# Performance work log

Measured on AMD Instinct MI355X. Metric: run time of the kernel, lower is better.

## Reference

```python
import jax, jax.numpy as jnp
import numpy as np

N_USERS = 100000
N_ITEMS = 50000
N_NODES = N_USERS + N_ITEMS  # 150000
N_EDGES = 1000000
N_INTENTS = 4
EMBED_K = 64
CHUNK = EMBED_K // N_INTENTS  # 16
N_LAYERS = 3


def setup_inputs() -> dict:
    key = jax.random.key(0)
    k1, k2, k3, k4 = jax.random.split(key, 4)
    Gu = jax.random.normal(k1, (N_USERS, EMBED_K), dtype=jnp.float32) * 0.1
    Gi = jax.random.normal(k2, (N_ITEMS, EMBED_K), dtype=jnp.float32) * 0.1
    edge_index = jax.random.randint(k3, (2, N_EDGES), 0, N_NODES, dtype=jnp.int64)
    edge_index_intents = jax.random.normal(k4, (N_INTENTS, N_EDGES), dtype=jnp.float32)
    return {"Gu": Gu, "Gi": Gi, "edge_index": edge_index,
            "edge_index_intents": edge_index_intents}


def dgcf_layer(x, row, col, edge_index_intents):
    # x: [N, K, C]; edge_index_intents: [K, E]
    w = jax.nn.softmax(edge_index_intents, axis=0).T  # [E, K]
    deg = (jax.ops.segment_sum(w, row, num_segments=N_NODES)
           + jax.ops.segment_sum(w, col, num_segments=N_NODES))  # [N, K]
    # deg^-0.5 with inf -> 0 (as in the torch code)
    dis = jnp.where(deg > 0, 1.0 / jnp.sqrt(jnp.maximum(deg, 1e-12)), 0.0)  # [N, K]
    norm = dis[row] * dis[col]  # [E, K]
    msg = norm[:, :, None] * x[row]  # [E, K, C] gather-multiply
    return jax.ops.segment_sum(msg, col, num_segments=N_NODES)  # scatter-add at targets


def reference(Gu, Gi, edge_index, edge_index_intents):
    row, col = edge_index[0], edge_index[1]
    # ego embeddings split into intent chunks: [N, K, C]
    x = jnp.concatenate([Gu, Gi], axis=0).reshape(N_NODES, N_INTENTS, CHUNK)
    for _ in range(N_LAYERS):
        x = dgcf_layer(x, row, col, edge_index_intents)
    return x
```

## Files before the change

### kernel.cpp

```cpp
#include <hip/hip_runtime.h>
#include <hip/hip_bf16.h>
#include <hip/hip_fp16.h>
#include <math.h>

#define N_USERS 100000
#define N_ITEMS 50000
#define N_NODES 150000
#define N_EDGES 1000000
#define N_GU_FLAT (N_USERS * 64)
#define N_ALL_FLAT (N_NODES * 64)
#define NBUCK 586
#define HPITCH (2 * NBUCK)
#define EPB 4096
#define NEB ((N_EDGES + EPB - 1) / EPB)
#define BCAP 2048
#define FIXS 16777216.0f

typedef __hip_bfloat16 bf16;
typedef unsigned short ushort_t;
typedef unsigned int uint_t;
typedef unsigned long long u64_t;

__device__ __forceinline__ ushort_t f2bs(float f) {
    bf16 h = __float2bfloat16(f);
    return *reinterpret_cast<ushort_t*>(&h);
}
__device__ __forceinline__ float lo2f(uint_t u) {
    float f; *reinterpret_cast<uint_t*>(&f) = u << 16; return f;
}
__device__ __forceinline__ float hi2f(uint_t u) {
    float f; *reinterpret_cast<uint_t*>(&f) = u & 0xFFFF0000u; return f;
}
__device__ __forceinline__ uint_t pack2(float a, float b) {
    return (uint_t)f2bs(a) | ((uint_t)f2bs(b) << 16);
}
__device__ __forceinline__ ushort_t f2hs(float f) {
    __half h = __float2half(f);
    return *reinterpret_cast<ushort_t*>(&h);
}
__device__ __forceinline__ float hs2f(ushort_t u) {
    __half h; *reinterpret_cast<ushort_t*>(&h) = u;
    return __half2float(h);
}
__device__ __forceinline__ int fix24(float w) {
    return (int)__float2int_rn(w * FIXS);
}

__global__ __launch_bounds__(1024) void s1_hist_cast(
        const int* __restrict__ ei,
        const float* __restrict__ Gu, const float* __restrict__ Gi,
        ushort_t* __restrict__ xG, uint_t* __restrict__ H, int gE) {
    int b = blockIdx.x;
    int t = threadIdx.x;
    if (b >= gE) {
        long base = ((long)(b - gE) * 1024 + t) * 4;
        if (base >= N_ALL_FLAT) return;
        float4 v = (base < N_GU_FLAT) ? *(const float4*)(Gu + base)
                                      : *(const float4*)(Gi + (base - N_GU_FLAT));
        uint2 o;
        o.x = pack2(v.x, v.y);
        o.y = pack2(v.z, v.w);
        *(uint2*)(xG + base) = o;
        return;
    }
    __shared__ uint_t h[HPITCH];
    for (int j = t; j < HPITCH; j += 1024) h[j] = 0;
    __syncthreads();
    int eb = b * EPB;
    int lim = min(EPB, N_EDGES - eb);
    for (int i = t; i < lim; i += 1024) {
        int e = eb + i;
        int r = ei[e];
        int c = ei[N_EDGES + e];
        atomicAdd(&h[c >> 8], 1u);
        atomicAdd(&h[NBUCK + (r >> 8)], 1u);
    }
    __syncthreads();
    for (int j = t; j < HPITCH; j += 1024) H[(size_t)b * HPITCH + j] = h[j];
}

__global__ __launch_bounds__(256) void s2_scan_blocks(
        const uint_t* __restrict__ H, uint_t* __restrict__ bases,
        uint_t* __restrict__ totals) {
    int j = blockIdx.x;
    int t = threadIdx.x;
    __shared__ uint_t s[256];
    uint_t v = (t < NEB) ? H[(size_t)t * HPITCH + j] : 0u;
    s[t] = v;
    __syncthreads();
    for (int off = 1; off < 256; off <<= 1) {
        uint_t a = (t >= off) ? s[t - off] : 0u;
        __syncthreads();
        s[t] += a;
        __syncthreads();
    }
    if (t < NEB) bases[(size_t)t * HPITCH + j] = s[t] - v;
    if (t == 255) totals[j] = s[255];
}

__global__ __launch_bounds__(1024) void s3_scatter(
        const int* __restrict__ ei, const float* __restrict__ intents,
        const uint_t* __restrict__ bases,
        uint_t* __restrict__ tmp_meta, u64_t* __restrict__ tmp_w,
        u64_t* __restrict__ tmp_row) {
    extern __shared__ char smem[];
    u64_t*  cw    = (u64_t*)smem;
    u64_t*  rw    = (u64_t*)(smem + 32768);
    uint_t* cmeta = (uint_t*)(smem + 65536);
    uint_t* cpos  = (uint_t*)(smem + 81920);
    uint_t* rpos  = (uint_t*)(smem + 98304);
    uint_t* ctr   = (uint_t*)(smem + 114688);
    uint_t* lexcl = (uint_t*)(smem + 119376);
    uint_t* stmp  = (uint_t*)(smem + 124064);
    int b = blockIdx.x, t = threadIdx.x;
    for (int j = t; j < HPITCH; j += 1024) ctr[j] = 0;
    __syncthreads();
    int eb = b * EPB;
    int lim = min(EPB, N_EDGES - eb);
    int  jcol[4], jrow[4];
    uint_t rkc[4], rkr[4], meta[4];
    u64_t cwv[4], rwv[4];
    bool val[4];
#pragma unroll
    for (int q = 0; q < 4; ++q) {
        int i = t + q * 1024;
        val[q] = (i < lim);
        int e = eb + (val[q] ? i : 0);
        int r = ei[e];
        int c = ei[N_EDGES + e];
        float v0 = intents[e];
        float v1 = intents[N_EDGES + e];
        float v2 = intents[2 * N_EDGES + e];
        float v3 = intents[3 * N_EDGES + e];
        float m  = fmaxf(fmaxf(v0, v1), fmaxf(v2, v3));
        float x0 = __expf(v0 - m), x1 = __expf(v1 - m);
        float x2 = __expf(v2 - m), x3 = __expf(v3 - m);
        float inv = 1.0f / (x0 + x1 + x2 + x3);
        float w0 = x0 * inv, w1 = x1 * inv, w2 = x2 * inv, w3 = x3 * inv;
        jcol[q] = c >> 8;
        jrow[q] = r >> 8;
        if (val[q]) {
            rkc[q] = atomicAdd(&ctr[jcol[q]], 1u);
            rkr[q] = atomicAdd(&ctr[NBUCK + jrow[q]], 1u);
        }
        meta[q] = ((uint_t)(c & 255) << 24) | (uint_t)r;
        cwv[q]  = (u64_t)pack2(w0, w1) | ((u64_t)pack2(w2, w3) << 32);
        rwv[q]  = (u64_t)f2hs(w0) | ((u64_t)f2hs(w1) << 16) |
                  ((u64_t)f2hs(w2) << 32) | ((u64_t)(uint_t)(r & 255) << 48);
    }
    __syncthreads();
    {
        uint_t v = (t < NBUCK) ? ctr[t] : 0u;
        stmp[t] = v;
        __syncthreads();
        for (int off = 1; off < 1024; off <<= 1) {
            uint_t a = (t >= off) ? stmp[t - off] : 0u;
            __syncthreads();
            stmp[t] += a;
            __syncthreads();
        }
        if (t < NBUCK) lexcl[t] = stmp[t] - v;
    }
    __syncthreads();
    {
        uint_t v = (t < NBUCK) ? ctr[NBUCK + t] : 0u;
        stmp[t] = v;
        __syncthreads();
        for (int off = 1; off < 1024; off <<= 1) {
            uint_t a = (t >= off) ? stmp[t - off] : 0u;
            __syncthreads();
            stmp[t] += a;
            __syncthreads();
        }
        if (t < NBUCK) lexcl[NBUCK + t] = stmp[t] - v;
    }
    __syncthreads();
#pragma unroll
    for (int q = 0; q < 4; ++q) {
        if (!val[q]) continue;
        uint_t lp = lexcl[jcol[q]] + rkc[q];
        cmeta[lp] = meta[q];
        cw[lp]    = cwv[q];
        cpos[lp]  = (uint_t)jcol[q] * BCAP + bases[(size_t)b * HPITCH + jcol[q]] + rkc[q];
        uint_t lr = lexcl[NBUCK + jrow[q]] + rkr[q];
        rw[lr]    = rwv[q];
        rpos[lr]  = (uint_t)jrow[q] * BCAP + bases[(size_t)b * HPITCH + NBUCK + jrow[q]] + rkr[q];
    }
    __syncthreads();
    for (int i = t; i < lim; i += 1024) {
        uint_t p = cpos[i];
        tmp_meta[p] = cmeta[i];
        tmp_w[p]    = cw[i];
        tmp_row[rpos[i]] = rw[i];
    }
}

__global__ __launch_bounds__(1024) void s4_finalize(
        const uint_t* __restrict__ tmp_meta, const u64_t* __restrict__ tmp_w,
        const u64_t* __restrict__ tmp_row, const uint_t* __restrict__ totals,
        uint_t* __restrict__ rec_src, int* __restrict__ offs_c, int* __restrict__ cnt_c,
        float* __restrict__ dis) {
    __shared__ uint_t meta_s[BCAP];
    __shared__ u64_t  w_s[BCAP];
    __shared__ u64_t  rw_s[BCAP];
    __shared__ uint_t hist[256], excl[256], run[256], sc[256];
    __shared__ int deg[1024];
    int b = blockIdx.x, t = threadIdx.x;
    if (t < 256) { hist[t] = 0u; run[t] = 0u; }
    deg[t] = 0;
    __syncthreads();
    uint_t c0 = (uint_t)b * BCAP;
    int nc = min((int)totals[b], BCAP);
    int nr = min((int)totals[NBUCK + b], BCAP);
    for (int i = t; i < nc; i += 1024) {
        meta_s[i] = tmp_meta[c0 + i];
        w_s[i]    = tmp_w[c0 + i];
    }
    for (int i = t; i < nr; i += 1024) rw_s[i] = tmp_row[c0 + i];
    __syncthreads();
    for (int i = t; i < nc; i += 1024) {
        uint_t nl = meta_s[i] >> 24;
        u64_t w = w_s[i];
        atomicAdd(&hist[nl], 1u);
        atomicAdd(&deg[nl * 4 + 0], fix24(lo2f((uint_t)w)));
        atomicAdd(&deg[nl * 4 + 1], fix24(hi2f((uint_t)w)));
        atomicAdd(&deg[nl * 4 + 2], fix24(lo2f((uint_t)(w >> 32))));
        atomicAdd(&deg[nl * 4 + 3], fix24(hi2f((uint_t)(w >> 32))));
    }
    for (int i = t; i < nr; i += 1024) {
        u64_t rv = rw_s[i];
        uint_t nl = (uint_t)(rv >> 48) & 255u;
        float w0 = hs2f((ushort_t)(rv & 0xFFFF));
        float w1 = hs2f((ushort_t)((rv >> 16) & 0xFFFF));
        float w2 = hs2f((ushort_t)((rv >> 32) & 0xFFFF));
        float w3 = 1.0f - w0 - w1 - w2;
        atomicAdd(&deg[nl * 4 + 0], fix24(w0));
        atomicAdd(&deg[nl * 4 + 1], fix24(w1));
        atomicAdd(&deg[nl * 4 + 2], fix24(w2));
        atomicAdd(&deg[nl * 4 + 3], fix24(w3));
    }
    __syncthreads();
    if (t < 256) sc[t] = hist[t];
    __syncthreads();
    for (int off = 1; off < 256; off <<= 1) {
        uint_t a = (t < 256 && t >= off) ? sc[t - off] : 0u;
        __syncthreads();
        if (t < 256) sc[t] += a;
        __syncthreads();
    }
    if (t < 256) excl[t] = sc[t] - hist[t];
    __syncthreads();
    for (int i = t; i < nc; i += 1024) {
        uint_t m = meta_s[i];
        uint_t nl = m >> 24;
        uint_t p = atomicAdd(&run[nl], 1u);
        rec_src[c0 + excl[nl] + p] = m & 0x00FFFFFFu;
    }
    if (t < 256) {
        int n = b * 256 + t;
        if (n < N_NODES) {
            offs_c[n] = (int)(c0 + excl[t]);
            cnt_c[n]  = (int)hist[t];
            float d0 = (float)deg[t * 4 + 0] * (1.0f / FIXS);
            float d1 = (float)deg[t * 4 + 1] * (1.0f / FIXS);
            float d2 = (float)deg[t * 4 + 2] * (1.0f / FIXS);
            float d3 = (float)deg[t * 4 + 3] * (1.0f / FIXS);
            float4 dd;
            dd.x = (d0 > 0.f) ? rsqrtf(fmaxf(d0, 1e-12f)) : 0.f;
            dd.y = (d1 > 0.f) ? rsqrtf(fmaxf(d1, 1e-12f)) : 0.f;
            dd.z = (d2 > 0.f) ? rsqrtf(fmaxf(d2, 1e-12f)) : 0.f;
            dd.w = (d3 > 0.f) ? rsqrtf(fmaxf(d3, 1e-12f)) : 0.f;
            *(float4*)(dis + (size_t)n * 4) = dd;
        }
    }
}

template <int MODE>
__global__ __launch_bounds__(256) void dg_agg(const ushort_t* __restrict__ xin,
                                              ushort_t* __restrict__ xout_b,
                                              float* __restrict__ xout_f,
                                              const uint_t* __restrict__ rec_src,
                                              const int* __restrict__ cnt_c,
                                              const int* __restrict__ offs_c,
                                              const float* __restrict__ dis) {
    int n = (blockIdx.x * 256 + threadIdx.x) >> 3;
    if (n >= N_NODES) return;
    int lane = threadIdx.x & 63;
    int j = lane & 7, k = j >> 1;
    int sg = lane & 56;
    int base = offs_c[n];
    int cnt  = cnt_c[n];
    float dd = dis[n * 4 + k];
    float a0 = 0.f, a1 = 0.f, a2 = 0.f, a3 = 0.f;
    float a4 = 0.f, a5 = 0.f, a6 = 0.f, a7 = 0.f;
    for (int c = 0; c < cnt; c += 8) {
        int idx = c + j;
        uint_t sv = (idx < cnt) ? rec_src[base + idx] : 0u;
        int srcs[8];
#pragma unroll
        for (int i = 0; i < 8; ++i) srcs[i] = (int)__shfl(sv, sg + i, 64);
#pragma unroll
        for (int i = 0; i < 8; ++i) {
            bool v = (c + i) < cnt;
            int src = v ? srcs[i] : srcs[0];
            float nk = v ? ((MODE == 0) ? dis[src * 4 + k] : 1.f) : 0.f;
            uint4 xu = *(const uint4*)(xin + (long)src * 64 + j * 8);
            a0 = fmaf(nk, lo2f(xu.x), a0); a1 = fmaf(nk, hi2f(xu.x), a1);
            a2 = fmaf(nk, lo2f(xu.y), a2); a3 = fmaf(nk, hi2f(xu.y), a3);
            a4 = fmaf(nk, lo2f(xu.z), a4); a5 = fmaf(nk, hi2f(xu.z), a5);
            a6 = fmaf(nk, lo2f(xu.w), a6); a7 = fmaf(nk, hi2f(xu.w), a7);
        }
    }
    float sc = (MODE == 2) ? dd : dd * dd;
    a0 *= sc; a1 *= sc; a2 *= sc; a3 *= sc;
    a4 *= sc; a5 *= sc; a6 *= sc; a7 *= sc;
    long o = (long)n * 64 + j * 8;
    if (MODE == 2) {
        *(float4*)(xout_f + o)     = make_float4(a0, a1, a2, a3);
        *(float4*)(xout_f + o + 4) = make_float4(a4, a5, a6, a7);
    } else {
        uint4 ob;
        ob.x = pack2(a0, a1); ob.y = pack2(a2, a3);
        ob.z = pack2(a4, a5); ob.w = pack2(a6, a7);
        *(uint4*)(xout_b + o) = ob;
    }
}

extern "C" void kernel_launch(void* const* d_in, const int* in_sizes, int n_in,
                              void* d_out, int out_size, void* d_ws, size_t ws_size,
                              hipStream_t stream) {
    const float* Gu      = (const float*)d_in[0];
    const float* Gi      = (const float*)d_in[1];
    const int*   ei      = (const int*)d_in[2];
    const float* intents = (const float*)d_in[3];
    float* out = (float*)d_out;

    char* ws = (char*)d_ws;
    size_t off = 0;
    int* offs_c = (int*)(ws + off);       off += (size_t)N_NODES * 4;
    int* cnt_c  = (int*)(ws + off);       off += (size_t)N_NODES * 4;
    float* dis  = (float*)(ws + off);     off += (size_t)N_NODES * 16;
    uint_t* rec_src = (uint_t*)(ws + off); off += (size_t)NBUCK * BCAP * 4;
    uint_t* totals   = (uint_t*)(ws + off); off += 8192;
    ushort_t* xG = (ushort_t*)(ws + off); off += (size_t)N_ALL_FLAT * 2;
    ushort_t* xA = (ushort_t*)(ws + off); off += (size_t)N_ALL_FLAT * 2;
    ushort_t* xB = (ushort_t*)(ws + off); off += (size_t)N_ALL_FLAT * 2;
    uint_t* tmp_meta = (uint_t*)xA;
    u64_t*  tmp_w    = (u64_t*)((char*)xA + (size_t)NBUCK * BCAP * 4);
    u64_t*  tmp_row  = (u64_t*)xB;
    uint_t* H     = (uint_t*)((char*)xB + (size_t)NBUCK * BCAP * 8);
    uint_t* bases = (uint_t*)((char*)xB + (size_t)NBUCK * BCAP * 8 + 1200000);
    (void)ws_size; (void)in_sizes; (void)n_in; (void)out_size;

    const int gE1 = NEB;
    const int gC1 = (N_ALL_FLAT / 4 + 1023) / 1024;

    s1_hist_cast<<<gE1 + gC1, 1024, 0, stream>>>(ei, Gu, Gi, xG, H, gE1);
    s2_scan_blocks<<<HPITCH, 256, 0, stream>>>(H, bases, totals);

    const size_t S3_LDS = 128160;
    hipFuncSetAttribute((const void*)s3_scatter,
                        hipFuncAttributeMaxDynamicSharedMemorySize, (int)S3_LDS);
    s3_scatter<<<NEB, 1024, S3_LDS, stream>>>(ei, intents, bases,
                                              tmp_meta, tmp_w, tmp_row);
    s4_finalize<<<NBUCK, 1024, 0, stream>>>(tmp_meta, tmp_w, tmp_row, totals,
                                            rec_src, offs_c, cnt_c, dis);

    int gAgg = (N_NODES * 8 + 255) / 256;
    dg_agg<0><<<gAgg, 256, 0, stream>>>(xG, xA, nullptr, rec_src, cnt_c, offs_c, dis);
    dg_agg<1><<<gAgg, 256, 0, stream>>>(xA, xB, nullptr, rec_src, cnt_c, offs_c, dis);
    dg_agg<2><<<gAgg, 256, 0, stream>>>(xB, nullptr, out, rec_src, cnt_c, offs_c, dis);
}
```

Before: 224.3 us.

## Replace histogram and scan passes with global atomic bucket reservation

Removes the separate per-block histogram kernel and cross-block scan kernel; each scatter block now reserves its slot range per bucket with one global atomicAdd per bucket, and the bf16 cast of the embeddings moves into the finalize kernel as extra blocks. This cuts two kernel launches and the H/bases round trip through memory. Edge order within a bucket becomes nondeterministic, so floating-point accumulation order in the later stages can vary between runs. A memset of the counters is added.

```diff
diff --git a/kernel.cpp b/kernel.cpp
--- a/kernel.cpp
+++ b/kernel.cpp
@@ -15,6 +15,7 @@
 #define NEB ((N_EDGES + EPB - 1) / EPB)
 #define BCAP 2048
 #define FIXS 16777216.0f
+#define GCAST ((N_ALL_FLAT / 4 + 1023) / 1024)
 
 typedef __hip_bfloat16 bf16;
 typedef unsigned short ushort_t;
@@ -46,61 +47,9 @@
     return (int)__float2int_rn(w * FIXS);
 }
 
-__global__ __launch_bounds__(1024) void s1_hist_cast(
-        const int* __restrict__ ei,
-        const float* __restrict__ Gu, const float* __restrict__ Gi,
-        ushort_t* __restrict__ xG, uint_t* __restrict__ H, int gE) {
-    int b = blockIdx.x;
-    int t = threadIdx.x;
-    if (b >= gE) {
-        long base = ((long)(b - gE) * 1024 + t) * 4;
-        if (base >= N_ALL_FLAT) return;
-        float4 v = (base < N_GU_FLAT) ? *(const float4*)(Gu + base)
-                                      : *(const float4*)(Gi + (base - N_GU_FLAT));
-        uint2 o;
-        o.x = pack2(v.x, v.y);
-        o.y = pack2(v.z, v.w);
-        *(uint2*)(xG + base) = o;
-        return;
-    }
-    __shared__ uint_t h[HPITCH];
-    for (int j = t; j < HPITCH; j += 1024) h[j] = 0;
-    __syncthreads();
-    int eb = b * EPB;
-    int lim = min(EPB, N_EDGES - eb);
-    for (int i = t; i < lim; i += 1024) {
-        int e = eb + i;
-        int r = ei[e];
-        int c = ei[N_EDGES + e];
-        atomicAdd(&h[c >> 8], 1u);
-        atomicAdd(&h[NBUCK + (r >> 8)], 1u);
-    }
-    __syncthreads();
-    for (int j = t; j < HPITCH; j += 1024) H[(size_t)b * HPITCH + j] = h[j];
-}
-
-__global__ __launch_bounds__(256) void s2_scan_blocks(
-        const uint_t* __restrict__ H, uint_t* __restrict__ bases,
-        uint_t* __restrict__ totals) {
-    int j = blockIdx.x;
-    int t = threadIdx.x;
-    __shared__ uint_t s[256];
-    uint_t v = (t < NEB) ? H[(size_t)t * HPITCH + j] : 0u;
-    s[t] = v;
-    __syncthreads();
-    for (int off = 1; off < 256; off <<= 1) {
-        uint_t a = (t >= off) ? s[t - off] : 0u;
-        __syncthreads();
-        s[t] += a;
-        __syncthreads();
-    }
-    if (t < NEB) bases[(size_t)t * HPITCH + j] = s[t] - v;
-    if (t == 255) totals[j] = s[255];
-}
-
 __global__ __launch_bounds__(1024) void s3_scatter(
         const int* __restrict__ ei, const float* __restrict__ intents,
-        const uint_t* __restrict__ bases,
+        uint_t* __restrict__ gctr,
         uint_t* __restrict__ tmp_meta, u64_t* __restrict__ tmp_w,
         u64_t* __restrict__ tmp_row) {
     extern __shared__ char smem[];
@@ -111,7 +60,8 @@
     uint_t* rpos  = (uint_t*)(smem + 98304);
     uint_t* ctr   = (uint_t*)(smem + 114688);
     uint_t* lexcl = (uint_t*)(smem + 119376);
-    uint_t* stmp  = (uint_t*)(smem + 124064);
+    uint_t* gb    = (uint_t*)(smem + 124064);
+    uint_t* stmp  = cpos;
     int b = blockIdx.x, t = threadIdx.x;
     for (int j = t; j < HPITCH; j += 1024) ctr[j] = 0;
     __syncthreads();
@@ -149,6 +99,8 @@
                   ((u64_t)f2hs(w2) << 32) | ((u64_t)(uint_t)(r & 255) << 48);
     }
     __syncthreads();
+    for (int j = t; j < HPITCH; j += 1024)
+        gb[j] = atomicAdd(&gctr[j], ctr[j]);
     {
         uint_t v = (t < NBUCK) ? ctr[t] : 0u;
         stmp[t] = v;
@@ -181,10 +133,10 @@
         uint_t lp = lexcl[jcol[q]] + rkc[q];
         cmeta[lp] = meta[q];
         cw[lp]    = cwv[q];
-        cpos[lp]  = (uint_t)jcol[q] * BCAP + bases[(size_t)b * HPITCH + jcol[q]] + rkc[q];
+        cpos[lp]  = (uint_t)jcol[q] * BCAP + gb[jcol[q]] + rkc[q];
         uint_t lr = lexcl[NBUCK + jrow[q]] + rkr[q];
         rw[lr]    = rwv[q];
-        rpos[lr]  = (uint_t)jrow[q] * BCAP + bases[(size_t)b * HPITCH + NBUCK + jrow[q]] + rkr[q];
+        rpos[lr]  = (uint_t)jrow[q] * BCAP + gb[NBUCK + jrow[q]] + rkr[q];
     }
     __syncthreads();
     for (int i = t; i < lim; i += 1024) {
@@ -197,7 +149,9 @@
 
 __global__ __launch_bounds__(1024) void s4_finalize(
         const uint_t* __restrict__ tmp_meta, const u64_t* __restrict__ tmp_w,
-        const u64_t* __restrict__ tmp_row, const uint_t* __restrict__ totals,
+        const u64_t* __restrict__ tmp_row, const uint_t* __restrict__ gctr,
+        const float* __restrict__ Gu, const float* __restrict__ Gi,
+        ushort_t* __restrict__ xG,
         uint_t* __restrict__ rec_src, int* __restrict__ offs_c, int* __restrict__ cnt_c,
         float* __restrict__ dis) {
     __shared__ uint_t meta_s[BCAP];
@@ -206,12 +160,23 @@
     __shared__ uint_t hist[256], excl[256], run[256], sc[256];
     __shared__ int deg[1024];
     int b = blockIdx.x, t = threadIdx.x;
+    if (b >= NBUCK) {
+        long base = ((long)(b - NBUCK) * 1024 + t) * 4;
+        if (base >= N_ALL_FLAT) return;
+        float4 v = (base < N_GU_FLAT) ? *(const float4*)(Gu + base)
+                                      : *(const float4*)(Gi + (base - N_GU_FLAT));
+        uint2 o;
+        o.x = pack2(v.x, v.y);
+        o.y = pack2(v.z, v.w);
+        *(uint2*)(xG + base) = o;
+        return;
+    }
     if (t < 256) { hist[t] = 0u; run[t] = 0u; }
     deg[t] = 0;
     __syncthreads();
     uint_t c0 = (uint_t)b * BCAP;
-    int nc = min((int)totals[b], BCAP);
-    int nr = min((int)totals[NBUCK + b], BCAP);
+    int nc = min((int)gctr[b], BCAP);
+    int nr = min((int)gctr[NBUCK + b], BCAP);
     for (int i = t; i < nc; i += 1024) {
         meta_s[i] = tmp_meta[c0 + i];
         w_s[i]    = tmp_w[c0 + i];
@@ -341,30 +306,25 @@
     int* cnt_c  = (int*)(ws + off);       off += (size_t)N_NODES * 4;
     float* dis  = (float*)(ws + off);     off += (size_t)N_NODES * 16;
     uint_t* rec_src = (uint_t*)(ws + off); off += (size_t)NBUCK * BCAP * 4;
-    uint_t* totals   = (uint_t*)(ws + off); off += 8192;
+    uint_t* gctr    = (uint_t*)(ws + off); off += 8192;
     ushort_t* xG = (ushort_t*)(ws + off); off += (size_t)N_ALL_FLAT * 2;
     ushort_t* xA = (ushort_t*)(ws + off); off += (size_t)N_ALL_FLAT * 2;
     ushort_t* xB = (ushort_t*)(ws + off); off += (size_t)N_ALL_FLAT * 2;
     uint_t* tmp_meta = (uint_t*)xA;
     u64_t*  tmp_w    = (u64_t*)((char*)xA + (size_t)NBUCK * BCAP * 4);
     u64_t*  tmp_row  = (u64_t*)xB;
-    uint_t* H     = (uint_t*)((char*)xB + (size_t)NBUCK * BCAP * 8);
-    uint_t* bases = (uint_t*)((char*)xB + (size_t)NBUCK * BCAP * 8 + 1200000);
     (void)ws_size; (void)in_sizes; (void)n_in; (void)out_size;
 
-    const int gE1 = NEB;
-    const int gC1 = (N_ALL_FLAT / 4 + 1023) / 1024;
-
-    s1_hist_cast<<<gE1 + gC1, 1024, 0, stream>>>(ei, Gu, Gi, xG, H, gE1);
-    s2_scan_blocks<<<HPITCH, 256, 0, stream>>>(H, bases, totals);
-
-    const size_t S3_LDS = 128160;
+    hipMemsetAsync(gctr, 0, HPITCH * sizeof(uint_t), stream);
+
+    const size_t S3_LDS = 128752;
     hipFuncSetAttribute((const void*)s3_scatter,
                         hipFuncAttributeMaxDynamicSharedMemorySize, (int)S3_LDS);
-    s3_scatter<<<NEB, 1024, S3_LDS, stream>>>(ei, intents, bases,
+    s3_scatter<<<NEB, 1024, S3_LDS, stream>>>(ei, intents, gctr,
                                               tmp_meta, tmp_w, tmp_row);
-    s4_finalize<<<NBUCK, 1024, 0, stream>>>(tmp_meta, tmp_w, tmp_row, totals,
-                                            rec_src, offs_c, cnt_c, dis);
+    s4_finalize<<<NBUCK + GCAST, 1024, 0, stream>>>(tmp_meta, tmp_w, tmp_row, gctr,
+                                                    Gu, Gi, xG,
+                                                    rec_src, offs_c, cnt_c, dis);
 
     int gAgg = (N_NODES * 8 + 255) / 256;
     dg_agg<0><<<gAgg, 256, 0, stream>>>(xG, xA, nullptr, rec_src, cnt_c, offs_c, dis);
```

After: 213.8 us. -4.7%, faster.
